# Kernel tuning notes

Hardware: AMD Instinct MI355X
Metric: run time of the kernel (lower is better)

## Reference

```python
import jax, jax.numpy as jnp
import numpy as np

EPS = 1e-5
B, L, D_MSA, D_PAIR = 1, 512, 256, 128
D_STATE, L0_IN, L0_OUT, EF = 32, 32, 32, 32
CV_IN, CV_OUT, C_HID = 3, 3, 32
TOP_K = 64
D_NODE_IN = D_MSA + 21 + D_STATE  # 309
D_INV = 2 * L0_IN + EF + 1 + CV_IN  # 100


def ln(x, g, b):
    mu = x.mean(-1, keepdims=True)
    var = ((x - mu) ** 2).mean(-1, keepdims=True)
    return (x - mu) * jax.lax.rsqrt(var + EPS) * g + b


def setup_inputs():
    key = jax.random.key(0)
    ks = iter(jax.random.split(key, 64))
    r = lambda *s: jax.random.normal(next(ks), s, jnp.float32)
    inp = {
        'xyz': r(B, L, 3, 3) * 3.0,
        'state': r(B, L, D_STATE),
        'atom_coor': r(B, L, 14, 3),
        'atom_feat': r(B, L, 14, 21),
        'msa': r(B, L, D_MSA),
        'pair': r(B, L, L, D_PAIR),
        'seq1hot': jax.random.uniform(next(ks), (B, L, 21)),
        'idx': jnp.arange(L, dtype=jnp.int32)[None].repeat(B, 0),
        'CA_atom_index': jax.random.randint(next(ks), (B, L), 0, 14),
        'top_k': TOP_K,
        # LayerNorm params
        'g_msa': jnp.ones(D_MSA), 'b_msa': jnp.zeros(D_MSA),
        'g_pair': jnp.ones(D_PAIR), 'b_pair': jnp.zeros(D_PAIR),
        'g_state': jnp.ones(D_STATE), 'b_state': jnp.zeros(D_STATE),
        'g_node': jnp.ones(L0_IN), 'b_node': jnp.zeros(L0_IN),
        'g_e1': jnp.ones(EF), 'b_e1': jnp.zeros(EF),
        # embeddings
        'Wx': r(D_NODE_IN, L0_IN) * 0.02, 'bx': jnp.zeros(L0_IN),
        'We1': r(D_PAIR, EF) * 0.02, 'be1': jnp.zeros(EF),
        # SE3-equivariant layer params
        'W1': r(D_INV, C_HID) * 0.1, 'b1': jnp.zeros(C_HID),
        'W2': r(L0_IN + C_HID, L0_OUT) * 0.1, 'b2': jnp.zeros(L0_OUT),
        'Wv': r(C_HID, 2 * CV_OUT) * 0.1,
        'Wvv': r(CV_IN, CV_OUT) * 0.3,
        'Wself': r(CV_IN, CV_OUT) * 0.3,
        # lddt head
        'Wl': r(L0_OUT, 1) * 0.1, 'bl': jnp.zeros(1),
    }
    return inp


def reference(xyz, state, atom_coor, atom_feat, msa, pair, seq1hot, idx,
              CA_atom_index, top_k, g_msa, b_msa, g_pair, b_pair, g_state,
              b_state, g_node, b_node, g_e1, b_e1, Wx, bx, We1, be1,
              W1, b1, W2, b2, Wv, Wvv, Wself, Wl, bl):
    Bb, Ll = msa.shape[:2]
    N = Bb * Ll
    # node / pair / state embeddings with fused LN+Linear chains
    node = ln(msa, g_msa, b_msa)
    pair_n = ln(pair, g_pair, b_pair)
    st = ln(state, g_state, b_state)
    node = jnp.concatenate([node, seq1hot, st], axis=-1)          # [B,L,309]
    node = ln(node @ Wx + bx, g_node, b_node)                      # [B,L,32]
    pair_e = ln(pair_n @ We1 + be1, g_e1, b_e1)                    # [B,L,L,32]

    # ---- make_graph_topk: kNN graph on CA coords ----
    CA = xyz[:, :, 1]                                              # [B,L,3]
    D = jnp.sqrt(jnp.sum((CA[:, :, None] - CA[:, None]) ** 2, -1) + 1e-8)
    D = D + 999.9 * jnp.eye(Ll, dtype=D.dtype)
    _, nbr = jax.lax.top_k(-D, top_k)                              # [B,L,k]
    src = jnp.repeat(jnp.arange(N), top_k)                         # [E]
    dst = (nbr + (jnp.arange(Bb) * Ll)[:, None, None]).reshape(-1) # [E]
    CAf = CA.reshape(N, 3)
    d_e = jax.lax.stop_gradient(CAf[dst] - CAf[src])               # [E,3] (detached as in torch)
    w_e = jnp.take_along_axis(pair_e.reshape(N, Ll, EF),
                              nbr.reshape(N, top_k, 1), axis=1).reshape(-1, EF)

    # ---- SE(3)-equivariant message passing (degree-0 + degree-1) ----
    l0 = node.reshape(N, -1)                                       # [N,32]
    v = (xyz - CA[:, :, None]).reshape(N, CV_IN, 3)                # [N,3,3]
    dn = jnp.linalg.norm(d_e, axis=-1, keepdims=True)              # [E,1]
    du = d_e / (dn + 1e-8)
    sv = jnp.einsum('eiv,ev->ei', v[src], du)                      # [E,3] invariants
    inv = jnp.concatenate([l0[src], l0[dst], w_e, dn, sv], -1)     # [E,100]
    m = jax.nn.gelu(inv @ W1 + b1)                                 # [E,32]
    agg = jax.ops.segment_sum(m, dst, num_segments=N)              # [N,32] scatter
    h_out = jnp.concatenate([l0, agg], -1) @ W2 + b2               # [N,32]
    coef = m @ Wv                                                  # [E,6]
    cd, cv = coef[:, :CV_OUT], coef[:, CV_OUT:]
    vproj = jnp.einsum('io,niv->nov', Wvv, v)                      # [N,3,3]
    vmsg = cd[:, :, None] * d_e[:, None] + cv[:, :, None] * vproj[src]
    v_agg = jax.ops.segment_sum(vmsg, dst, num_segments=N)         # [N,3,3]
    v_out = jnp.einsum('io,niv->nov', Wself, v) + v_agg            # [N,3,3]

    # ---- assemble refined coordinates ----
    state_o = h_out.reshape(Bb, Ll, -1)
    offset = v_out.reshape(Bb, Ll, -1, 3)
    CA_new = CA + offset[:, :, 1]
    CA_set = jnp.repeat(CA_new[:, :, None], 3, axis=2)
    CA_set = CA_set.at[:, 0:1].set(0.0)
    xyz_new = (offset + CA_set).reshape(Bb * Ll * 3, 3)
    lddt = jax.nn.sigmoid(ln(state_o, g_state, b_state) @ Wl + bl)
    return xyz_new, lddt
```

## Files before the change

kernel.cpp:

```cpp
#include <hip/hip_runtime.h>
#include <hip/hip_bf16.h>
#include <math.h>

typedef __hip_bfloat16 bf16;

__device__ __forceinline__ bool detect_bf16(const void* ones_vec) {
  return ((const unsigned int*)ones_vec)[0] == 0x3F803F80u;
}
__device__ __forceinline__ float ldf(const void* p, long idx, bool isb) {
  if (isb) return __bfloat162float(((const bf16*)p)[idx]);
  return ((const float*)p)[idx];
}
__device__ __forceinline__ void stf(void* p, long idx, float v, bool isb) {
  if (isb) ((bf16*)p)[idx] = __float2bfloat16(v);
  else     ((float*)p)[idx] = v;
}
__device__ __forceinline__ float wsum64(float x) {
#pragma unroll
  for (int off = 32; off > 0; off >>= 1) x += __shfl_xor(x, off, 64);
  return x;
}
__device__ __forceinline__ float wsum32(float x) {
#pragma unroll
  for (int off = 16; off > 0; off >>= 1) x += __shfl_xor(x, off, 64);
  return x;
}

__global__ __launch_bounds__(256) void k_node_topk(
    const void* __restrict__ xyz, const void* __restrict__ state,
    const void* __restrict__ msa, const void* __restrict__ seq1hot,
    const void* __restrict__ g_msa, const void* __restrict__ b_msa,
    const void* __restrict__ g_state, const void* __restrict__ b_state,
    const void* __restrict__ g_node, const void* __restrict__ b_node,
    const void* __restrict__ Wx, const void* __restrict__ bx,
    const void* __restrict__ Wvv,
    float* __restrict__ l0, float* __restrict__ CA, float* __restrict__ v,
    float* __restrict__ vproj, float* __restrict__ agg, float* __restrict__ v_agg,
    int* __restrict__ nbr)
{
  const bool isb = detect_bf16(g_msa);
  const int i = blockIdx.x;
  const int t = threadIdx.x;
  const int lane = t & 63, w = t >> 6;
  __shared__ float nin[312];
  __shared__ float wred[2][4];
  __shared__ float part[8][32];
  __shared__ float sxyz[9], sv9[9];
  __shared__ float cx[512], cy[512], cz[512];
  __shared__ unsigned long long key[512];

  for (int tt = t; tt < 512; tt += 256) {
    cx[tt] = ldf(xyz, tt * 9 + 3, isb);
    cy[tt] = ldf(xyz, tt * 9 + 4, isb);
    cz[tt] = ldf(xyz, tt * 9 + 5, isb);
  }

  float x = ldf(msa, i * 256 + t, isb);
  float s1 = wsum64(x), s2 = wsum64(x * x);
  if (lane == 0) { wred[0][w] = s1; wred[1][w] = s2; }
  if (t < 9) sxyz[t] = ldf(xyz, i * 9 + t, isb);
  __syncthreads();
  float S  = wred[0][0] + wred[0][1] + wred[0][2] + wred[0][3];
  float Sq = wred[1][0] + wred[1][1] + wred[1][2] + wred[1][3];
  float mu = S * (1.f / 256.f);
  float rs = rsqrtf(fmaxf(Sq * (1.f / 256.f) - mu * mu, 0.f) + 1e-5f);
  nin[t] = (x - mu) * rs * ldf(g_msa, t, isb) + ldf(b_msa, t, isb);
  if (t < 21) nin[256 + t] = ldf(seq1hot, i * 21 + t, isb);
  if (t < 3)  nin[309 + t] = 0.f;

  if (w == 0) {
    float sx  = (lane < 32) ? ldf(state, i * 32 + lane, isb) : 0.f;
    float Ss  = wsum64(sx), Ssq = wsum64(sx * sx);
    float mus = Ss * (1.f / 32.f);
    float rss = rsqrtf(fmaxf(Ssq * (1.f / 32.f) - mus * mus, 0.f) + 1e-5f);
    if (lane < 32)
      nin[277 + lane] = (sx - mus) * rss * ldf(g_state, lane, isb) + ldf(b_state, lane, isb);
  }
  __syncthreads();

  const int c = t & 31, g = t >> 5;
  float acc = 0.f;
  for (int f = g; f < 309; f += 8) acc += nin[f] * ldf(Wx, f * 32 + c, isb);
  part[g][c] = acc;

  float xi = cx[i], yi = cy[i], zi = cz[i];
  for (int tt = t; tt < 512; tt += 256) {
    float dx = cx[tt] - xi, dy = cy[tt] - yi, dz = cz[tt] - zi;
    float d2 = dx * dx + dy * dy + dz * dz;
    unsigned int bits = (tt == i) ? 0x7f800000u : __float_as_uint(d2);
    key[tt] = ((unsigned long long)bits << 32) | (unsigned int)tt;
  }
  __syncthreads();

  if (w == 0) {
    float a = 0.f;
    if (lane < 32) {
      a = ldf(bx, lane, isb);
#pragma unroll
      for (int gg = 0; gg < 8; ++gg) a += part[gg][lane];
    }
    float Sa = wsum32(a), Saq = wsum32(a * a);
    float mn = Sa * (1.f / 32.f);
    float rn = rsqrtf(fmaxf(Saq * (1.f / 32.f) - mn * mn, 0.f) + 1e-5f);
    if (lane < 32)
      l0[i * 32 + lane] = (a - mn) * rn * ldf(g_node, lane, isb) + ldf(b_node, lane, isb);
  } else if (w == 1) {
    if (lane < 3) CA[i * 3 + lane] = sxyz[3 + lane];
    if (lane < 9) {
      float vv = sxyz[lane] - sxyz[3 + lane % 3];
      v[i * 9 + lane] = vv;
      sv9[lane] = vv;
    }
    if (lane < 32) agg[i * 32 + lane] = 0.f;
  } else if (w == 2) {
    if (lane < 9) v_agg[i * 9 + lane] = 0.f;
  }
  __syncthreads();
  if (w == 1 && lane < 9) {
    int o = lane / 3, xc = lane % 3;
    float s = 0.f;
#pragma unroll
    for (int ii = 0; ii < 3; ++ii) s += ldf(Wvv, ii * 3 + o, isb) * sv9[ii * 3 + xc];
    vproj[i * 9 + lane] = s;
  }

  for (int k = 2; k <= 512; k <<= 1) {
    for (int j = k >> 1; j > 0; j >>= 1) {
      __syncthreads();
      int tt  = threadIdx.x;
      int i0 = ((tt & ~(j - 1)) << 1) | (tt & (j - 1));
      int i1 = i0 | j;
      bool up = ((i0 & k) == 0);
      unsigned long long a = key[i0], b = key[i1];
      if ((a > b) == up) { key[i0] = b; key[i1] = a; }
    }
  }
  __syncthreads();
  if (threadIdx.x < 64)
    nbr[i * 64 + threadIdx.x] = (int)(key[threadIdx.x] & 0xffffffffu);
}

__global__ __launch_bounds__(256) void k_edge(
    const void* __restrict__ pair,
    const void* __restrict__ g_pair, const void* __restrict__ b_pair,
    const void* __restrict__ We1, const void* __restrict__ be1,
    const void* __restrict__ g_e1, const void* __restrict__ b_e1,
    const void* __restrict__ W1, const void* __restrict__ b1,
    const void* __restrict__ Wv,
    const int* __restrict__ nbr,
    const float* __restrict__ l0, const float* __restrict__ CA,
    const float* __restrict__ v, const float* __restrict__ vproj,
    float* __restrict__ agg, float* __restrict__ v_agg)
{
  const bool isb = detect_bf16(g_pair);
  __shared__ float WT[32][132];
  __shared__ float ped[16][132];
  __shared__ float sinvL[16][68];
  __shared__ float mL[16][33];
  __shared__ float coefL[16][8];
  __shared__ float geoE[16][4];
  __shared__ float gpl[128], bpl[128];
  __shared__ float partA[8][33];
  __shared__ float a1b[32];
  __shared__ float sgeo[21];
  __shared__ float wvL[6][33];
  __shared__ int   jnL[16];

  const int i  = blockIdx.x >> 2;
  const int qt = blockIdx.x & 3;
  const int t  = threadIdx.x;
  const int e  = t >> 4;
  const int q  = t & 15;
  const int c  = t & 31;
  const int rg = t >> 5;

  const int jn = nbr[i * 64 + qt * 16 + e];
  if (q == 0) jnL[e] = jn;

  float4 pA, pB;
  {
    const size_t base = ((size_t)(i * 512 + jn)) * 128 + q * 8;
    if (isb) {
      pA.x = ldf(pair, base + 0, true); pA.y = ldf(pair, base + 1, true);
      pA.z = ldf(pair, base + 2, true); pA.w = ldf(pair, base + 3, true);
      pB.x = ldf(pair, base + 4, true); pB.y = ldf(pair, base + 5, true);
      pB.z = ldf(pair, base + 6, true); pB.w = ldf(pair, base + 7, true);
    } else {
      const float4* p4 = (const float4*)pair;
      pA = p4[base >> 2]; pB = p4[(base >> 2) + 1];
    }
  }

  if (t < 128) gpl[t] = ldf(g_pair, t, isb);
  else         bpl[t - 128] = ldf(b_pair, t - 128, isb);
  for (int idx = t; idx < 4096; idx += 256) {
    int cc = idx & 31, k = idx >> 5;
    int slot = ((k >> 2) + 4 * (cc & 7)) & 31;
    WT[cc][slot * 4 + (k & 3)] = ldf(We1, idx, isb);
  }
  {
    int kk = q * 2;
    const float2 lj = *(const float2*)&l0[jn * 32 + kk];
    sinvL[e][kk] = lj.x; sinvL[e][kk + 1] = lj.y;
  }
  if (t < 3)       sgeo[t] = CA[i * 3 + t];
  else if (t < 12) sgeo[t] = v[i * 9 + (t - 3)];
  else if (t < 21) sgeo[t] = vproj[i * 9 + (t - 12)];
  if (t < 192) wvL[t % 6][t / 6] = ldf(Wv, t, isb);
  {
    const int fg = t >> 5;
    float p = 0.f;
#pragma unroll
    for (int k = 0; k < 4; ++k) {
      int f = 4 * fg + k;
      p += l0[i * 32 + f] * ldf(W1, f * 32 + c, isb);
    }
    partA[fg][c] = p;
  }

  float S  = pA.x + pA.y + pA.z + pA.w + pB.x + pB.y + pB.z + pB.w;
  float Sq = pA.x * pA.x + pA.y * pA.y + pA.z * pA.z + pA.w * pA.w
           + pB.x * pB.x + pB.y * pB.y + pB.z * pB.z + pB.w * pB.w;
#pragma unroll
  for (int off = 8; off > 0; off >>= 1) {
    S  += __shfl_xor(S,  off, 64);
    Sq += __shfl_xor(Sq, off, 64);
  }
  __syncthreads();

  if (t < 32) {
    float b = ldf(b1, t, isb);
#pragma unroll
    for (int gg = 0; gg < 8; ++gg) b += partA[gg][t];
    a1b[t] = b;
  }

  {
    float mu = S * (1.f / 128.f);
    float rs = rsqrtf(fmaxf(Sq * (1.f / 128.f) - mu * mu, 0.f) + 1e-5f);
    float4 g0 = *(const float4*)&gpl[q * 8], g1 = *(const float4*)&gpl[q * 8 + 4];
    float4 b0 = *(const float4*)&bpl[q * 8], b1v = *(const float4*)&bpl[q * 8 + 4];
    float4 o0, o1;
    o0.x = (pA.x - mu) * rs * g0.x + b0.x;
    o0.y = (pA.y - mu) * rs * g0.y + b0.y;
    o0.z = (pA.z - mu) * rs * g0.z + b0.z;
    o0.w = (pA.w - mu) * rs * g0.w + b0.w;
    o1.x = (pB.x - mu) * rs * g1.x + b1v.x;
    o1.y = (pB.y - mu) * rs * g1.y + b1v.y;
    o1.z = (pB.z - mu) * rs * g1.z + b1v.z;
    o1.w = (pB.w - mu) * rs * g1.w + b1v.w;
    *(float4*)&ped[e][q * 8]     = o0;
    *(float4*)&ped[e][q * 8 + 4] = o1;
  }
  if (t < 16) {
    int j = jnL[t];
    float dex = CA[j * 3 + 0] - sgeo[0];
    float dey = CA[j * 3 + 1] - sgeo[1];
    float dez = CA[j * 3 + 2] - sgeo[2];
    float dn  = sqrtf(dex * dex + dey * dey + dez * dez);
    float idn = 1.f / (dn + 1e-8f);
    float dux = dex * idn, duy = dey * idn, duz = dez * idn;
    sinvL[t][64] = dn;
    sinvL[t][65] = sgeo[3] * dux + sgeo[4] * duy + sgeo[5] * duz;
    sinvL[t][66] = sgeo[6] * dux + sgeo[7] * duy + sgeo[8] * duz;
    sinvL[t][67] = sgeo[9] * dux + sgeo[10] * duy + sgeo[11] * duz;
    geoE[t][0] = dex; geoE[t][1] = dey; geoE[t][2] = dez;
  }
  __syncthreads();

  const int e0 = rg * 2, e1i = rg * 2 + 1;
  const int rot = 4 * (c & 7);
  float A0 = ldf(be1, c, isb), A1 = A0;
#pragma unroll 4
  for (int k4 = 0; k4 < 32; ++k4) {
    float4 wf = *(const float4*)&WT[c][((k4 + rot) & 31) << 2];
    float4 p0 = *(const float4*)&ped[e0][k4 << 2];
    float4 p1 = *(const float4*)&ped[e1i][k4 << 2];
    A0 += p0.x * wf.x + p0.y * wf.y + p0.z * wf.z + p0.w * wf.w;
    A1 += p1.x * wf.x + p1.y * wf.y + p1.z * wf.z + p1.w * wf.w;
  }
  {
    const float ge1c = ldf(g_e1, c, isb), bee1c = ldf(b_e1, c, isb);
    float S0 = wsum32(A0), Q0 = wsum32(A0 * A0);
    float S1 = wsum32(A1), Q1 = wsum32(A1 * A1);
    float mu0 = S0 * (1.f / 32.f);
    float r0  = rsqrtf(fmaxf(Q0 * (1.f / 32.f) - mu0 * mu0, 0.f) + 1e-5f);
    float mu1 = S1 * (1.f / 32.f);
    float r1  = rsqrtf(fmaxf(Q1 * (1.f / 32.f) - mu1 * mu1, 0.f) + 1e-5f);
    sinvL[e0][32 + c]  = (A0 - mu0) * r0 * ge1c + bee1c;
    sinvL[e1i][32 + c] = (A1 - mu1) * r1 * ge1c + bee1c;
  }
  __syncthreads();

  for (int idx = t; idx < 2176; idx += 256) {
    int cc = idx & 31, k = idx >> 5;
    int slot = ((k >> 2) + 4 * (cc & 7)) & 31;
    WT[cc][slot * 4 + (k & 3)] = ldf(W1, (32 + k) * 32 + cc, isb);
  }
  __syncthreads();

  {
    float M0 = a1b[c], M1 = M0;
#pragma unroll 4
    for (int k4 = 0; k4 < 17; ++k4) {
      float4 wf = *(const float4*)&WT[c][((k4 + rot) & 31) << 2];
      float4 s0 = *(const float4*)&sinvL[e0][k4 << 2];
      float4 s1 = *(const float4*)&sinvL[e1i][k4 << 2];
      M0 += s0.x * wf.x + s0.y * wf.y + s0.z * wf.z + s0.w * wf.w;
      M1 += s1.x * wf.x + s1.y * wf.y + s1.z * wf.z + s1.w * wf.w;
    }
    float u0 = 0.7978845608028654f * (M0 + 0.044715f * M0 * M0 * M0);
    float g0 = 0.5f * M0 * (1.f + tanhf(u0));
    float u1 = 0.7978845608028654f * (M1 + 0.044715f * M1 * M1 * M1);
    float g1 = 0.5f * M1 * (1.f + tanhf(u1));
    mL[e0][c] = g0;  mL[e1i][c] = g1;
    atomicAdd(&agg[jnL[e0] * 32 + c], g0);
    atomicAdd(&agg[jnL[e1i] * 32 + c], g1);
  }
  __syncthreads();

  if (t < 96) {
    int ee = t / 6, o = t - ee * 6;
    float s = 0.f;
#pragma unroll 8
    for (int cc = 0; cc < 32; ++cc) s += mL[ee][cc] * wvL[o][cc];
    coefL[ee][o] = s;
  }
  __syncthreads();
  if (t < 144) {
    int ee = t / 9, l = t - ee * 9, o = l / 3, x = l - o * 3;
    float val = coefL[ee][o] * geoE[ee][x] + coefL[ee][3 + o] * sgeo[12 + o * 3 + x];
    atomicAdd(&v_agg[jnL[ee] * 9 + l], val);
  }
}

__global__ __launch_bounds__(64) void k_out(
    const float* __restrict__ l0, const float* __restrict__ agg,
    const float* __restrict__ v, const float* __restrict__ v_agg,
    const float* __restrict__ CA,
    const void* __restrict__ W2, const void* __restrict__ b2,
    const void* __restrict__ Wself,
    const void* __restrict__ g_state, const void* __restrict__ b_state,
    const void* __restrict__ Wl, const void* __restrict__ bl,
    void* __restrict__ out)
{
  const bool isb = detect_bf16(g_state);
  const int l = blockIdx.x;
  const int lane = threadIdx.x;
  const int c = lane & 31, h = lane >> 5;
  __shared__ float scat[64], soff[9];
  if (lane < 32) { scat[lane] = l0[l * 32 + lane]; scat[32 + lane] = agg[l * 32 + lane]; }
  __syncthreads();

  float acc = 0.f;
  {
    const int fb = h * 32;
    for (int f = 0; f < 32; ++f) acc += scat[fb + f] * ldf(W2, (fb + f) * 32 + c, isb);
  }
  acc += __shfl_xor(acc, 32, 64);
  acc += ldf(b2, c, isb);

  float mu = wsum32(acc) * (1.f / 32.f);
  float rs = rsqrtf(fmaxf(wsum32(acc * acc) * (1.f / 32.f) - mu * mu, 0.f) + 1e-5f);
  float hn = (acc - mu) * rs * ldf(g_state, c, isb) + ldf(b_state, c, isb);
  float pre = wsum32(hn * ldf(Wl, c, isb)) + ldf(bl, 0, isb);
  if (lane == 0) stf(out, 4608 + l, 1.f / (1.f + expf(-pre)), isb);

  if (lane < 9) {
    int o = lane / 3, xx = lane % 3;
    float s = v_agg[l * 9 + lane];
#pragma unroll
    for (int ii = 0; ii < 3; ++ii) s += ldf(Wself, ii * 3 + o, isb) * v[l * 9 + ii * 3 + xx];
    soff[lane] = s;
  }
  __syncthreads();
  if (lane < 9) {
    int xx = lane % 3;
    float add = (l == 0) ? 0.f : (CA[l * 3 + xx] + soff[3 + xx]);
    stf(out, l * 9 + lane, soff[lane] + add, isb);
  }
}

extern "C" void kernel_launch(void* const* d_in, const int* in_sizes, int n_in,
                              void* d_out, int out_size, void* d_ws, size_t ws_size,
                              hipStream_t stream) {
  (void)in_sizes; (void)n_in; (void)out_size; (void)ws_size;
  const void* xyz     = d_in[0];
  const void* state   = d_in[1];
  const void* msa     = d_in[4];
  const void* pair    = d_in[5];
  const void* seq1hot = d_in[6];
  const void* g_msa   = d_in[10];
  const void* b_msa   = d_in[11];
  const void* g_pair  = d_in[12];
  const void* b_pair  = d_in[13];
  const void* g_state = d_in[14];
  const void* b_state = d_in[15];
  const void* g_node  = d_in[16];
  const void* b_node  = d_in[17];
  const void* g_e1    = d_in[18];
  const void* b_e1    = d_in[19];
  const void* Wx      = d_in[20];
  const void* bx      = d_in[21];
  const void* We1     = d_in[22];
  const void* be1     = d_in[23];
  const void* W1      = d_in[24];
  const void* b1      = d_in[25];
  const void* W2      = d_in[26];
  const void* b2      = d_in[27];
  const void* Wv      = d_in[28];
  const void* Wvv     = d_in[29];
  const void* Wself   = d_in[30];
  const void* Wl      = d_in[31];
  const void* bl      = d_in[32];

  float* ws    = (float*)d_ws;
  float* l0    = ws;
  float* CA    = ws + 16384;
  float* v     = ws + 17920;
  float* vproj = ws + 22528;
  float* agg   = ws + 27136;
  float* v_agg = ws + 43520;
  int*   nbr   = (int*)(ws + 48128);

  hipLaunchKernelGGL(k_node_topk, dim3(512), dim3(256), 0, stream,
                     xyz, state, msa, seq1hot, g_msa, b_msa, g_state, b_state,
                     g_node, b_node, Wx, bx, Wvv, l0, CA, v, vproj, agg, v_agg, nbr);
  hipLaunchKernelGGL(k_edge, dim3(2048), dim3(256), 0, stream,
                     pair, g_pair, b_pair, We1, be1, g_e1, b_e1, W1, b1, Wv,
                     nbr, l0, CA, v, vproj, agg, v_agg);
  hipLaunchKernelGGL(k_out, dim3(512), dim3(64), 0, stream,
                     l0, agg, v, v_agg, CA, W2, b2, Wself, g_state, b_state, Wl, bl,
                     (void*)d_out);
}
```

Baseline: 292.9 us.

## Keep We1 in registers and split K per half-wave to drop block barriers

The pair-edge projection now keeps the We1 weights in registers: each thread holds 64 values for its half of the K dimension, and the two half-waves' partial sums are combined with a cross-lane shuffle. Each wave handles its own four edges end to end, so the shared-memory We1 staging and two `__syncthreads` barriers go away. The W1 tile is loaded into shared memory up front instead of after the edge LayerNorm, and the b1 bias reduction is done per thread. The cost is much higher register pressure, which may lower occupancy, plus redundant per-thread global weight loads.

Measured after the change: 338.0 us. 1.15x slower.

```diff
diff --git a/kernel.cpp b/kernel.cpp
--- a/kernel.cpp
+++ b/kernel.cpp
@@ -161,7 +161,6 @@
   __shared__ float geoE[16][4];
   __shared__ float gpl[128], bpl[128];
   __shared__ float partA[8][33];
-  __shared__ float a1b[32];
   __shared__ float sgeo[21];
   __shared__ float wvL[6][33];
   __shared__ int   jnL[16];
@@ -172,7 +171,9 @@
   const int e  = t >> 4;
   const int q  = t & 15;
   const int c  = t & 31;
-  const int rg = t >> 5;
+  const int w  = t >> 6;
+  const int lane = t & 63;
+  const int h  = lane >> 5;
 
   const int jn = nbr[i * 64 + qt * 16 + e];
   if (q == 0) jnL[e] = jn;
@@ -191,12 +192,18 @@
     }
   }
 
+  float we1r[64];
+#pragma unroll
+  for (int kk = 0; kk < 64; ++kk) we1r[kk] = ldf(We1, (h * 64 + kk) * 32 + c, isb);
+  const float be1c = ldf(be1, c, isb), ge1c = ldf(g_e1, c, isb);
+  const float bee1c = ldf(b_e1, c, isb);
+
   if (t < 128) gpl[t] = ldf(g_pair, t, isb);
   else         bpl[t - 128] = ldf(b_pair, t - 128, isb);
-  for (int idx = t; idx < 4096; idx += 256) {
+  for (int idx = t; idx < 2176; idx += 256) {
     int cc = idx & 31, k = idx >> 5;
     int slot = ((k >> 2) + 4 * (cc & 7)) & 31;
-    WT[cc][slot * 4 + (k & 3)] = ldf(We1, idx, isb);
+    WT[cc][slot * 4 + (k & 3)] = ldf(W1, (32 + k) * 32 + cc, isb);
   }
   {
     int kk = q * 2;
@@ -227,13 +234,6 @@
     Sq += __shfl_xor(Sq, off, 64);
   }
   __syncthreads();
-
-  if (t < 32) {
-    float b = ldf(b1, t, isb);
-#pragma unroll
-    for (int gg = 0; gg < 8; ++gg) b += partA[gg][t];
-    a1b[t] = b;
-  }
 
   {
     float mu = S * (1.f / 128.f);
@@ -252,55 +252,64 @@
     *(float4*)&ped[e][q * 8]     = o0;
     *(float4*)&ped[e][q * 8 + 4] = o1;
   }
-  if (t < 16) {
-    int j = jnL[t];
+  if (lane < 4) {
+    const int eg = (w << 2) + lane;
+    const int j = jnL[eg];
     float dex = CA[j * 3 + 0] - sgeo[0];
     float dey = CA[j * 3 + 1] - sgeo[1];
     float dez = CA[j * 3 + 2] - sgeo[2];
     float dn  = sqrtf(dex * dex + dey * dey + dez * dez);
     float idn = 1.f / (dn + 1e-8f);
     float dux = dex * idn, duy = dey * idn, duz = dez * idn;
-    sinvL[t][64] = dn;
-    sinvL[t][65] = sgeo[3] * dux + sgeo[4] * duy + sgeo[5] * duz;
-    sinvL[t][66] = sgeo[6] * dux + sgeo[7] * duy + sgeo[8] * duz;
-    sinvL[t][67] = sgeo[9] * dux + sgeo[10] * duy + sgeo[11] * duz;
-    geoE[t][0] = dex; geoE[t][1] = dey; geoE[t][2] = dez;
-  }
-  __syncthreads();
-
-  const int e0 = rg * 2, e1i = rg * 2 + 1;
-  const int rot = 4 * (c & 7);
-  float A0 = ldf(be1, c, isb), A1 = A0;
+    sinvL[eg][64] = dn;
+    sinvL[eg][65] = sgeo[3] * dux + sgeo[4] * duy + sgeo[5] * duz;
+    sinvL[eg][66] = sgeo[6] * dux + sgeo[7] * duy + sgeo[8] * duz;
+    sinvL[eg][67] = sgeo[9] * dux + sgeo[10] * duy + sgeo[11] * duz;
+    geoE[eg][0] = dex; geoE[eg][1] = dey; geoE[eg][2] = dez;
+  }
+
+  const int ew = w << 2;
+  float A0 = 0.f, A1 = 0.f, A2 = 0.f, A3 = 0.f;
+  {
+    const int kb = h * 64;
 #pragma unroll 4
-  for (int k4 = 0; k4 < 32; ++k4) {
-    float4 wf = *(const float4*)&WT[c][((k4 + rot) & 31) << 2];
-    float4 p0 = *(const float4*)&ped[e0][k4 << 2];
-    float4 p1 = *(const float4*)&ped[e1i][k4 << 2];
-    A0 += p0.x * wf.x + p0.y * wf.y + p0.z * wf.z + p0.w * wf.w;
-    A1 += p1.x * wf.x + p1.y * wf.y + p1.z * wf.z + p1.w * wf.w;
-  }
-  {
-    const float ge1c = ldf(g_e1, c, isb), bee1c = ldf(b_e1, c, isb);
-    float S0 = wsum32(A0), Q0 = wsum32(A0 * A0);
-    float S1 = wsum32(A1), Q1 = wsum32(A1 * A1);
-    float mu0 = S0 * (1.f / 32.f);
-    float r0  = rsqrtf(fmaxf(Q0 * (1.f / 32.f) - mu0 * mu0, 0.f) + 1e-5f);
-    float mu1 = S1 * (1.f / 32.f);
-    float r1  = rsqrtf(fmaxf(Q1 * (1.f / 32.f) - mu1 * mu1, 0.f) + 1e-5f);
-    sinvL[e0][32 + c]  = (A0 - mu0) * r0 * ge1c + bee1c;
-    sinvL[e1i][32 + c] = (A1 - mu1) * r1 * ge1c + bee1c;
-  }
-  __syncthreads();
-
-  for (int idx = t; idx < 2176; idx += 256) {
-    int cc = idx & 31, k = idx >> 5;
-    int slot = ((k >> 2) + 4 * (cc & 7)) & 31;
-    WT[cc][slot * 4 + (k & 3)] = ldf(W1, (32 + k) * 32 + cc, isb);
-  }
-  __syncthreads();
-
-  {
-    float M0 = a1b[c], M1 = M0;
+    for (int k4 = 0; k4 < 16; ++k4) {
+      const int ko = kb + (k4 << 2);
+      float4 p0 = *(const float4*)&ped[ew + 0][ko];
+      float4 p1 = *(const float4*)&ped[ew + 1][ko];
+      float4 p2 = *(const float4*)&ped[ew + 2][ko];
+      float4 p3 = *(const float4*)&ped[ew + 3][ko];
+      float w0 = we1r[4 * k4], w1 = we1r[4 * k4 + 1];
+      float w2 = we1r[4 * k4 + 2], w3 = we1r[4 * k4 + 3];
+      A0 += p0.x * w0 + p0.y * w1 + p0.z * w2 + p0.w * w3;
+      A1 += p1.x * w0 + p1.y * w1 + p1.z * w2 + p1.w * w3;
+      A2 += p2.x * w0 + p2.y * w1 + p2.z * w2 + p2.w * w3;
+      A3 += p3.x * w0 + p3.y * w1 + p3.z * w2 + p3.w * w3;
+    }
+  }
+  {
+    float a0 = A0 + __shfl_xor(A0, 32, 64) + be1c;
+    float a1 = A1 + __shfl_xor(A1, 32, 64) + be1c;
+    float a2 = A2 + __shfl_xor(A2, 32, 64) + be1c;
+    float a3 = A3 + __shfl_xor(A3, 32, 64) + be1c;
+#pragma unroll
+    for (int rr = 0; rr < 4; ++rr) {
+      float a = (rr == 0) ? a0 : ((rr == 1) ? a1 : ((rr == 2) ? a2 : a3));
+      float Sr = wsum32(a), Qr = wsum32(a * a);
+      float mur = Sr * (1.f / 32.f);
+      float rr2 = rsqrtf(fmaxf(Qr * (1.f / 32.f) - mur * mur, 0.f) + 1e-5f);
+      if (h == 0) sinvL[ew + rr][32 + c] = (a - mur) * rr2 * ge1c + bee1c;
+    }
+  }
+
+  {
+    float a1c = ldf(b1, c, isb);
+#pragma unroll
+    for (int gg = 0; gg < 8; ++gg) a1c += partA[gg][c];
+
+    const int e0 = ew + 2 * h, e1i = e0 + 1;
+    const int rot = 4 * (c & 7);
+    float M0 = a1c, M1 = a1c;
 #pragma unroll 4
     for (int k4 = 0; k4 < 17; ++k4) {
       float4 wf = *(const float4*)&WT[c][((k4 + rot) & 31) << 2];
```
